# Optimization experiments

Hardware: AMD Instinct MI355X
Metric: run time of the kernel (lower is better)

Reference implementation:

```python
import jax, jax.numpy as jnp
import numpy as np

IN_F = 128
OUT_F = 128
N_LAYER = 2
DEPTH = 9                       # tree depth -> levels 0..DEPTH-1
N_TREES = 128
TREE_SIZE = 2 ** DEPTH - 1      # 511 nodes per complete binary tree
N = N_TREES * TREE_SIZE         # 65408 total nodes
E = N_TREES * (TREE_SIZE - 1)   # 65280 parent->child edges


def _build_forest():
    """Complete binary trees in heap layout; leaves get order 0, root order DEPTH-1."""
    k = np.arange(TREE_SIZE)
    depth = np.floor(np.log2(k + 1)).astype(np.int32)
    order_tree = (DEPTH - 1) - depth                      # per-node level within a tree
    node_order = np.tile(order_tree, N_TREES).astype(np.int32)
    internal = k[k < 2 ** (DEPTH - 1) - 1]                # internal nodes have 2 children
    par = np.repeat(internal, 2)
    chi = np.empty_like(par)
    chi[0::2] = 2 * internal + 1
    chi[1::2] = 2 * internal + 2
    eorder_tree = order_tree[par]
    offs = (np.arange(N_TREES) * TREE_SIZE)[:, None]
    parents = (par[None, :] + offs).reshape(-1)
    children = (chi[None, :] + offs).reshape(-1)
    adjacency = np.stack([parents, children], axis=1).astype(np.int32)
    edge_order = np.tile(eorder_tree, N_TREES).astype(np.int32)
    return node_order, adjacency, edge_order


def setup_inputs() -> dict:
    key = jax.random.key(0)
    ks = jax.random.split(key, 8)
    node_order, adjacency, edge_order = _build_forest()
    s = 0.05
    return {
        "features": jax.random.normal(ks[0], (N, IN_F), jnp.float32),
        "W_iou": jax.random.normal(ks[1], (N_LAYER, 3 * OUT_F, IN_F), jnp.float32) * s,
        "b_iou": jax.random.normal(ks[2], (N_LAYER, 3 * OUT_F), jnp.float32) * s,
        "U_iou": jax.random.normal(ks[3], (N_LAYER, 3 * OUT_F, OUT_F), jnp.float32) * s,
        "W_f": jax.random.normal(ks[4], (N_LAYER, OUT_F, IN_F), jnp.float32) * s,
        "b_f": jax.random.normal(ks[5], (N_LAYER, OUT_F), jnp.float32) * s,
        "U_f": jax.random.normal(ks[6], (N_LAYER, OUT_F, OUT_F), jnp.float32) * s,
        "node_order": jnp.asarray(node_order),
        "adjacency_list": jnp.asarray(adjacency),
        "edge_order": jnp.asarray(edge_order),
        "treesizes": jnp.full((N_TREES,), TREE_SIZE, jnp.int32),
        "n_levels": DEPTH,
    }


def reference(features, W_iou, b_iou, U_iou, W_f, b_f, U_f,
              node_order, adjacency_list, edge_order, treesizes, n_levels):
    n_nodes = features.shape[0]
    parent = adjacency_list[:, 0]
    child = adjacency_list[:, 1]
    n_trees = treesizes.shape[0]
    tree_size = n_nodes // n_trees
    # root of each (equal-sized) tree = argmax of node_order within its segment
    root_idx = (jnp.argmax(node_order.reshape(n_trees, tree_size), axis=1)
                + jnp.arange(n_trees) * tree_size)

    def run_layer(Wi, bi, Ui, Wf, bf, Uf):
        Wx_iou = features @ Wi.T + bi              # [N, 3H], level-independent
        Wfx = features[parent] @ Wf.T + bf         # [E, H], per-edge forget input
        H = Wi.shape[0] // 3

        def step(carry, lvl):
            h, c = carry
            em = (edge_order == lvl).astype(features.dtype)[:, None]   # [E,1]
            ch = h[child]                                              # gather child h
            cc = c[child]
            h_sum = jax.ops.segment_sum(ch * em, parent, num_segments=n_nodes)
            iou = Wx_iou + h_sum @ Ui.T
            i_, o_, u_ = jnp.split(iou, 3, axis=1)
            i_ = jax.nn.sigmoid(i_)
            o_ = jax.nn.sigmoid(o_)
            u_ = jnp.tanh(u_)
            f = jax.nn.sigmoid(Wfx + ch @ Uf.T)                        # [E,H]
            c_sum = jax.ops.segment_sum(f * cc * em, parent, num_segments=n_nodes)
            c_new = i_ * u_ + c_sum
            h_new = o_ * jnp.tanh(c_new)
            nm = (node_order == lvl)[:, None]
            return (jnp.where(nm, h_new, h), jnp.where(nm, c_new, c)), None

        init = (jnp.zeros((n_nodes, H), features.dtype),
                jnp.zeros((n_nodes, H), features.dtype))
        (h, c), _ = jax.lax.scan(step, init, jnp.arange(n_levels))
        return h[root_idx], c[root_idx]

    f_h, f_c = jax.vmap(run_layer)(W_iou, b_iou, U_iou, W_f, b_f, U_f)
    return f_h, f_c
```

## Files before the change

### kernel.cpp

```cpp
#include <hip/hip_runtime.h>
#include <hip/hip_bf16.h>


#define TS 511
#define NT 128
#define NN (NT * TS)

typedef __attribute__((ext_vector_type(8))) short short8;
typedef __attribute__((ext_vector_type(4))) float floatx4;

#define MFMA_B16 __builtin_amdgcn_mfma_f32_16x16x32_bf16

#define BARLDS() do { \
    asm volatile("s_waitcnt lgkmcnt(0)" ::: "memory"); \
    __builtin_amdgcn_s_barrier(); \
    asm volatile("" ::: "memory"); \
} while (0)

__device__ __forceinline__ unsigned short f2b(float f) {
    return __builtin_bit_cast(unsigned short, __float2bfloat16(f));
}
__device__ __forceinline__ float b2f_u(unsigned short u) {
    unsigned v = (unsigned)u << 16;
    return __builtin_bit_cast(float, v);
}
__device__ __forceinline__ float rcp_(float x) { return __builtin_amdgcn_rcpf(x); }
__device__ __forceinline__ float sig_(float x) { return rcp_(1.0f + __expf(-x)); }
__device__ __forceinline__ float tanh_(float x) {
    float a = fabsf(x);
    float t = __expf(-2.0f * a);
    return copysignf((1.0f - t) * rcp_(1.0f + t), x);
}

__global__ void pack_b(const float* __restrict__ Wiou, const float* __restrict__ biou,
                       const float* __restrict__ Uiou, const float* __restrict__ Wf,
                       const float* __restrict__ bfv, const float* __restrict__ Uf,
                       const float* __restrict__ feat,
                       unsigned short* __restrict__ BgU, unsigned short* __restrict__ BgX,
                       float* __restrict__ bp5, unsigned short* __restrict__ xb) {
    int tid = blockIdx.x * 256 + threadIdx.x;
    if (tid < 1280) {
        int l = tid / 640, r = tid % 640, g = r >> 7, o = r & 127;
        bp5[tid] = (g < 3) ? biou[l * 384 + r] : bfv[l * 128 + o];
    }
    if (tid < 131072) {
        int l = tid >> 16, r = tid & 65535, col = r >> 7, kp = r & 127;
        float v = (col < 384) ? Uiou[(l * 384 + col) * 128 + kp]
                              : Uf[(l * 128 + (col - 384)) * 128 + kp];
        BgU[((size_t)(l * 512 + col)) * 128 + kp] = f2b(v);
    } else if (tid < 262144) {
        int e2 = tid - 131072;
        int l = e2 >> 16, r = e2 & 65535, col = r >> 7, kp = r & 127;
        float v = (col < 384) ? Wiou[(l * 384 + col) * 128 + kp]
                              : Wf[(l * 128 + (col - 384)) * 128 + kp];
        BgX[((size_t)(l * 512 + col)) * 128 + kp] = f2b(v);
    } else {
        int e = tid - 262144;
        size_t base = (size_t)e * 8;
        float4 v0 = *(const float4*)(feat + base);
        float4 v1 = *(const float4*)(feat + base + 4);
        short8 r;
        r[0] = (short)f2b(v0.x); r[1] = (short)f2b(v0.y);
        r[2] = (short)f2b(v0.z); r[3] = (short)f2b(v0.w);
        r[4] = (short)f2b(v1.x); r[5] = (short)f2b(v1.y);
        r[6] = (short)f2b(v1.z); r[7] = (short)f2b(v1.w);
        *(short8*)(xb + base) = r;
    }
}

__global__ __launch_bounds__(512, 2) void forest(
        const unsigned short* __restrict__ xb16, const unsigned short* __restrict__ BgU,
        const unsigned short* __restrict__ BgX, const float* __restrict__ bp5,
        float* __restrict__ out) {
    __shared__ __align__(16) unsigned short S[69632];
    const int HC0 = 26112;

    const int tid = threadIdx.x;
    const int l = blockIdx.x >> 7, tree = blockIdx.x & 127;
    const int lane = tid & 63, w = tid >> 6;
    const int quad = lane >> 4, l15 = lane & 15;
    const int o = w * 16 + l15;
    const unsigned short* xb = xb16 + (size_t)tree * TS * 128;
    const unsigned short* BU = BgU + (size_t)l * 512 * 128;
    const unsigned short* BX = BgX + (size_t)l * 512 * 128;

    short8 bU[4][4], bX[4][4];
#pragma unroll
    for (int g = 0; g < 4; g++) {
        const size_t cb = (size_t)(g * 128 + o) * 128;
#pragma unroll
        for (int kbl = 0; kbl < 4; kbl++) {
            bU[g][kbl] = *(const short8*)(BU + cb + kbl * 32 + quad * 8);
            bX[g][kbl] = *(const short8*)(BX + cb + kbl * 32 + quad * 8);
        }
    }
    float bb[5];
#pragma unroll
    for (int g = 0; g < 5; g++) bb[g] = bp5[l * 640 + g * 128 + o];

    auto ldx = [&](int heap, int kbl) -> short8 {
        return *(const short8*)(xb + (size_t)heap * 128 + kbl * 32 + quad * 8);
    };

    auto ltile = [&](int heapA, int selfH, int selfC) {
        floatx4 ai = (floatx4){0.f, 0.f, 0.f, 0.f};
        floatx4 ao = ai, au = ai;
#pragma unroll
        for (int kbl = 0; kbl < 4; kbl++) {
            short8 ax = ldx(heapA, kbl);
            ai = MFMA_B16(ax, bX[0][kbl], ai, 0, 0, 0);
            ao = MFMA_B16(ax, bX[1][kbl], ao, 0, 0, 0);
            au = MFMA_B16(ax, bX[2][kbl], au, 0, 0, 0);
        }
#pragma unroll
        for (int r = 0; r < 4; r++) {
            int idx = quad * 4 + r;
            float iv = sig_(ai[r] + bb[0]);
            float ov = sig_(ao[r] + bb[1]);
            float uv = tanh_(au[r] + bb[2]);
            float cn = iv * uv;
            float hn = ov * tanh_(cn);
            S[(selfH + idx) * 136 + o] = f2b(hn);
            S[HC0 + (selfC + idx) * 136 + o] = f2b(cn);
        }
    };

    auto itile = [&](int heapA, int chAh, int selfRB, int chRBc,
                     int nValid, bool isRoot) {
        floatx4 ai = (floatx4){0.f, 0.f, 0.f, 0.f};
        floatx4 ao = ai, au = ai, awx = ai, af0 = ai, af1 = ai;
#pragma unroll
        for (int kbl = 0; kbl < 4; kbl++) {
            short8 h0 = *(const short8*)&S[chAh * 136 + kbl * 32 + quad * 8];
            short8 h1 = *(const short8*)&S[(chAh + 1) * 136 + kbl * 32 + quad * 8];
            short8 ax = ldx(heapA, kbl);
            ai = MFMA_B16(h0, bU[0][kbl], ai, 0, 0, 0);
            ai = MFMA_B16(h1, bU[0][kbl], ai, 0, 0, 0);
            ao = MFMA_B16(h0, bU[1][kbl], ao, 0, 0, 0);
            ao = MFMA_B16(h1, bU[1][kbl], ao, 0, 0, 0);
            au = MFMA_B16(h0, bU[2][kbl], au, 0, 0, 0);
            au = MFMA_B16(h1, bU[2][kbl], au, 0, 0, 0);
            af0 = MFMA_B16(h0, bU[3][kbl], af0, 0, 0, 0);
            af1 = MFMA_B16(h1, bU[3][kbl], af1, 0, 0, 0);
            ai = MFMA_B16(ax, bX[0][kbl], ai, 0, 0, 0);
            ao = MFMA_B16(ax, bX[1][kbl], ao, 0, 0, 0);
            au = MFMA_B16(ax, bX[2][kbl], au, 0, 0, 0);
            awx = MFMA_B16(ax, bX[3][kbl], awx, 0, 0, 0);
        }
#pragma unroll
        for (int r = 0; r < 4; r++) {
            int idx = quad * 4 + r;
            if (idx < nValid) {
                float iv = sig_(ai[r] + bb[0]);
                float ov = sig_(ao[r] + bb[1]);
                float uv = tanh_(au[r] + bb[2]);
                float f0 = sig_(awx[r] + af0[r] + bb[3]);
                float f1 = sig_(awx[r] + af1[r] + bb[4]);
                float c0 = b2f_u(S[HC0 + (chRBc + 2 * idx) * 136 + o]);
                float c1 = b2f_u(S[HC0 + (chRBc + 2 * idx + 1) * 136 + o]);
                float cn = iv * uv + f0 * c0 + f1 * c1;
                float hn = ov * tanh_(cn);
                S[(selfRB + idx) * 136 + o] = f2b(hn);
                S[HC0 + (selfRB + idx) * 136 + o] = f2b(cn);
                if (isRoot) {
                    out[((size_t)l * 128 + tree) * 128 + o] = hn;
                    out[32768 + ((size_t)l * 128 + tree) * 128 + o] = cn;
                }
            }
        }
    };

#pragma unroll
    for (int s = 0; s < 2; s++)
        ltile(255 + s * 16 + l15, 384 + s * 16, 256 + s * 16);
    BARLDS();

#pragma unroll 2
    for (int t = 0; t < 8; t++) {
        if (t < 7) {
            int b2 = (t + 1) & 1;
#pragma unroll
            for (int s = 0; s < 2; s++)
                ltile(255 + (t + 1) * 32 + s * 16 + l15,
                      384 + b2 * 32 + s * 16, 256 + b2 * 32 + s * 16);
        }
        int b = t & 1;
        itile(127 + t * 16 + l15,
              384 + b * 32 + 2 * l15,
              t * 16,
              256 + b * 32,
              16, false);
        BARLDS();
    }

#pragma unroll
    for (int dd = 6; dd >= 0; dd--) {
        const int nd = 1 << dd;
        const int selfB = (dd == 6) ? 128 : 64 - 2 * nd;
        const int chB = (dd == 6) ? 0 : ((dd == 5) ? 128 : 64 - 4 * nd);
        const int mts = (nd + 15) >> 4;
#pragma unroll
        for (int mt = 0; mt < mts; mt++) {
            int rl = mt * 16 + l15;
            if (rl > nd - 1) rl = nd - 1;
            int nv = nd - mt * 16;
            if (nv > 16) nv = 16;
            itile(nd - 1 + rl,
                  chB + 2 * rl,
                  selfB + mt * 16,
                  chB + 2 * mt * 16,
                  nv, dd == 0);
        }
        BARLDS();
    }
}

extern "C" void kernel_launch(void* const* d_in, const int* in_sizes, int n_in,
                              void* d_out, int out_size, void* d_ws, size_t ws_size,
                              hipStream_t stream) {
    const float* feat = (const float*)d_in[0];
    const float* Wiou = (const float*)d_in[1];
    const float* biou = (const float*)d_in[2];
    const float* Uiou = (const float*)d_in[3];
    const float* Wf   = (const float*)d_in[4];
    const float* bfv  = (const float*)d_in[5];
    const float* Uf   = (const float*)d_in[6];
    float* out = (float*)d_out;

    unsigned short* BgU = (unsigned short*)d_ws;
    unsigned short* BgX = BgU + (size_t)131072;
    unsigned short* xb16 = BgX + (size_t)131072;
    float* bp5 = (float*)(xb16 + (size_t)NN * 128);

    pack_b<<<5112, 256, 0, stream>>>(Wiou, biou, Uiou, Wf, bfv, Uf, feat,
                                     BgU, BgX, bp5, xb16);
    forest<<<256, 512, 0, stream>>>(xb16, BgU, BgX, bp5, out);
}
```

Baseline: 157.6 us.

## Spill depth-7 states to global memory to shrink LDS footprint

The 128 depth-7 node h/c states are now written to a global scratch buffer instead of LDS, and depth 6 reads them back from global. This shrinks LDS use from about 136KB to about 69KB per block and uses a heap-indexed LDS layout for the upper levels. The launch-bound occupancy hint is dropped. The cost is extra global round trips plus a threadfence. With only 256 blocks the grid may not gain much from the smaller LDS footprint.

Result: slower. 206.0 us (+30.7%).

```diff
diff --git a/kernel.cpp b/kernel.cpp
--- a/kernel.cpp
+++ b/kernel.cpp
@@ -68,12 +68,13 @@
     }
 }
 
-__global__ __launch_bounds__(512, 2) void forest(
+__global__ __launch_bounds__(512) void forest(
         const unsigned short* __restrict__ xb16, const unsigned short* __restrict__ BgU,
         const unsigned short* __restrict__ BgX, const float* __restrict__ bp5,
+        unsigned short* __restrict__ hb7, unsigned short* __restrict__ cb7,
         float* __restrict__ out) {
-    __shared__ __align__(16) unsigned short S[69632];
-    const int HC0 = 26112;
+    __shared__ __align__(16) unsigned short S[34544];
+    const int HC0 = 17272;
 
     const int tid = threadIdx.x;
     const int l = blockIdx.x >> 7, tree = blockIdx.x & 127;
@@ -81,6 +82,8 @@
     const int quad = lane >> 4, l15 = lane & 15;
     const int o = w * 16 + l15;
     const unsigned short* xb = xb16 + (size_t)tree * TS * 128;
+    unsigned short* lh = hb7 + ((size_t)(l * 128 + tree)) * 128 * 128;
+    unsigned short* lc = cb7 + ((size_t)(l * 128 + tree)) * 128 * 128;
     const unsigned short* BU = BgU + (size_t)l * 512 * 128;
     const unsigned short* BX = BgX + (size_t)l * 512 * 128;
 
@@ -102,7 +105,7 @@
         return *(const short8*)(xb + (size_t)heap * 128 + kbl * 32 + quad * 8);
     };
 
-    auto ltile = [&](int heapA, int selfH, int selfC) {
+    auto ltile = [&](int heapA, int selfR) {
         floatx4 ai = (floatx4){0.f, 0.f, 0.f, 0.f};
         floatx4 ao = ai, au = ai;
 #pragma unroll
@@ -120,20 +123,20 @@
             float uv = tanh_(au[r] + bb[2]);
             float cn = iv * uv;
             float hn = ov * tanh_(cn);
-            S[(selfH + idx) * 136 + o] = f2b(hn);
-            S[HC0 + (selfC + idx) * 136 + o] = f2b(cn);
-        }
-    };
-
-    auto itile = [&](int heapA, int chAh, int selfRB, int chRBc,
-                     int nValid, bool isRoot) {
+            S[(selfR + idx) * 136 + o] = f2b(hn);
+            S[HC0 + (selfR + idx) * 136 + o] = f2b(cn);
+        }
+    };
+
+    auto d7g = [&](int t, int b) {
+        const int chAh = 63 + b * 32 + 2 * l15;
         floatx4 ai = (floatx4){0.f, 0.f, 0.f, 0.f};
         floatx4 ao = ai, au = ai, awx = ai, af0 = ai, af1 = ai;
 #pragma unroll
         for (int kbl = 0; kbl < 4; kbl++) {
             short8 h0 = *(const short8*)&S[chAh * 136 + kbl * 32 + quad * 8];
             short8 h1 = *(const short8*)&S[(chAh + 1) * 136 + kbl * 32 + quad * 8];
-            short8 ax = ldx(heapA, kbl);
+            short8 ax = ldx(127 + 16 * t + l15, kbl);
             ai = MFMA_B16(h0, bU[0][kbl], ai, 0, 0, 0);
             ai = MFMA_B16(h1, bU[0][kbl], ai, 0, 0, 0);
             ao = MFMA_B16(h0, bU[1][kbl], ao, 0, 0, 0);
@@ -150,18 +153,103 @@
 #pragma unroll
         for (int r = 0; r < 4; r++) {
             int idx = quad * 4 + r;
-            if (idx < nValid) {
+            float iv = sig_(ai[r] + bb[0]);
+            float ov = sig_(ao[r] + bb[1]);
+            float uv = tanh_(au[r] + bb[2]);
+            float f0 = sig_(awx[r] + af0[r] + bb[3]);
+            float f1 = sig_(awx[r] + af1[r] + bb[4]);
+            float c0 = b2f_u(S[HC0 + (63 + b * 32 + 2 * idx) * 136 + o]);
+            float c1 = b2f_u(S[HC0 + (63 + b * 32 + 2 * idx + 1) * 136 + o]);
+            float cn = iv * uv + f0 * c0 + f1 * c1;
+            float hn = ov * tanh_(cn);
+            size_t gi = (size_t)(t * 16 + idx) * 128 + o;
+            lh[gi] = f2b(hn);
+            lc[gi] = f2b(cn);
+        }
+    };
+
+    auto d6g = [&](int j) {
+        const int di0 = 32 * j + 2 * l15;
+        floatx4 ai = (floatx4){0.f, 0.f, 0.f, 0.f};
+        floatx4 ao = ai, au = ai, awx = ai, af0 = ai, af1 = ai;
+#pragma unroll
+        for (int kbl = 0; kbl < 4; kbl++) {
+            short8 h0 = *(const short8*)(lh + (size_t)di0 * 128 + kbl * 32 + quad * 8);
+            short8 h1 = *(const short8*)(lh + (size_t)(di0 + 1) * 128 + kbl * 32 + quad * 8);
+            short8 ax = ldx(63 + 16 * j + l15, kbl);
+            ai = MFMA_B16(h0, bU[0][kbl], ai, 0, 0, 0);
+            ai = MFMA_B16(h1, bU[0][kbl], ai, 0, 0, 0);
+            ao = MFMA_B16(h0, bU[1][kbl], ao, 0, 0, 0);
+            ao = MFMA_B16(h1, bU[1][kbl], ao, 0, 0, 0);
+            au = MFMA_B16(h0, bU[2][kbl], au, 0, 0, 0);
+            au = MFMA_B16(h1, bU[2][kbl], au, 0, 0, 0);
+            af0 = MFMA_B16(h0, bU[3][kbl], af0, 0, 0, 0);
+            af1 = MFMA_B16(h1, bU[3][kbl], af1, 0, 0, 0);
+            ai = MFMA_B16(ax, bX[0][kbl], ai, 0, 0, 0);
+            ao = MFMA_B16(ax, bX[1][kbl], ao, 0, 0, 0);
+            au = MFMA_B16(ax, bX[2][kbl], au, 0, 0, 0);
+            awx = MFMA_B16(ax, bX[3][kbl], awx, 0, 0, 0);
+        }
+#pragma unroll
+        for (int r = 0; r < 4; r++) {
+            int idx = quad * 4 + r;
+            int node = 63 + 16 * j + idx;
+            int dic = 32 * j + 2 * idx;
+            float iv = sig_(ai[r] + bb[0]);
+            float ov = sig_(ao[r] + bb[1]);
+            float uv = tanh_(au[r] + bb[2]);
+            float f0 = sig_(awx[r] + af0[r] + bb[3]);
+            float f1 = sig_(awx[r] + af1[r] + bb[4]);
+            float c0 = b2f_u(lc[(size_t)dic * 128 + o]);
+            float c1 = b2f_u(lc[(size_t)(dic + 1) * 128 + o]);
+            float cn = iv * uv + f0 * c0 + f1 * c1;
+            float hn = ov * tanh_(cn);
+            S[node * 136 + o] = f2b(hn);
+            S[HC0 + node * 136 + o] = f2b(cn);
+        }
+    };
+
+    auto itile_l = [&](int base, int nv, bool isRoot) {
+        const int rl = (l15 < nv) ? l15 : nv - 1;
+        const int nA = base + rl;
+        const int ch0 = 2 * nA + 1;
+        floatx4 ai = (floatx4){0.f, 0.f, 0.f, 0.f};
+        floatx4 ao = ai, au = ai, awx = ai, af0 = ai, af1 = ai;
+#pragma unroll
+        for (int kbl = 0; kbl < 4; kbl++) {
+            short8 h0 = *(const short8*)&S[ch0 * 136 + kbl * 32 + quad * 8];
+            short8 h1 = *(const short8*)&S[(ch0 + 1) * 136 + kbl * 32 + quad * 8];
+            short8 ax = ldx(nA, kbl);
+            ai = MFMA_B16(h0, bU[0][kbl], ai, 0, 0, 0);
+            ai = MFMA_B16(h1, bU[0][kbl], ai, 0, 0, 0);
+            ao = MFMA_B16(h0, bU[1][kbl], ao, 0, 0, 0);
+            ao = MFMA_B16(h1, bU[1][kbl], ao, 0, 0, 0);
+            au = MFMA_B16(h0, bU[2][kbl], au, 0, 0, 0);
+            au = MFMA_B16(h1, bU[2][kbl], au, 0, 0, 0);
+            af0 = MFMA_B16(h0, bU[3][kbl], af0, 0, 0, 0);
+            af1 = MFMA_B16(h1, bU[3][kbl], af1, 0, 0, 0);
+            ai = MFMA_B16(ax, bX[0][kbl], ai, 0, 0, 0);
+            ao = MFMA_B16(ax, bX[1][kbl], ao, 0, 0, 0);
+            au = MFMA_B16(ax, bX[2][kbl], au, 0, 0, 0);
+            awx = MFMA_B16(ax, bX[3][kbl], awx, 0, 0, 0);
+        }
+#pragma unroll
+        for (int r = 0; r < 4; r++) {
+            int idx = quad * 4 + r;
+            if (idx < nv) {
+                int node = base + idx;
+                int ch = 2 * node + 1;
                 float iv = sig_(ai[r] + bb[0]);
                 float ov = sig_(ao[r] + bb[1]);
                 float uv = tanh_(au[r] + bb[2]);
                 float f0 = sig_(awx[r] + af0[r] + bb[3]);
                 float f1 = sig_(awx[r] + af1[r] + bb[4]);
-                float c0 = b2f_u(S[HC0 + (chRBc + 2 * idx) * 136 + o]);
-                float c1 = b2f_u(S[HC0 + (chRBc + 2 * idx + 1) * 136 + o]);
+                float c0 = b2f_u(S[HC0 + ch * 136 + o]);
+                float c1 = b2f_u(S[HC0 + (ch + 1) * 136 + o]);
                 float cn = iv * uv + f0 * c0 + f1 * c1;
                 float hn = ov * tanh_(cn);
-                S[(selfRB + idx) * 136 + o] = f2b(hn);
-                S[HC0 + (selfRB + idx) * 136 + o] = f2b(cn);
+                S[node * 136 + o] = f2b(hn);
+                S[HC0 + node * 136 + o] = f2b(cn);
                 if (isRoot) {
                     out[((size_t)l * 128 + tree) * 128 + o] = hn;
                     out[32768 + ((size_t)l * 128 + tree) * 128 + o] = cn;
@@ -170,49 +258,40 @@
         }
     };
 
-#pragma unroll
-    for (int s = 0; s < 2; s++)
-        ltile(255 + s * 16 + l15, 384 + s * 16, 256 + s * 16);
-    BARLDS();
-
-#pragma unroll 2
+    ltile(255 + l15, 63);
+    ltile(271 + l15, 63 + 16);
+    BARLDS();
+
+#pragma unroll 1
     for (int t = 0; t < 8; t++) {
+        const int b = t & 1;
         if (t < 7) {
-            int b2 = (t + 1) & 1;
-#pragma unroll
-            for (int s = 0; s < 2; s++)
-                ltile(255 + (t + 1) * 32 + s * 16 + l15,
-                      384 + b2 * 32 + s * 16, 256 + b2 * 32 + s * 16);
-        }
-        int b = t & 1;
-        itile(127 + t * 16 + l15,
-              384 + b * 32 + 2 * l15,
-              t * 16,
-              256 + b * 32,
-              16, false);
+            const int b2 = b ^ 1;
+            ltile(287 + 32 * t + l15, 63 + b2 * 32);
+            ltile(303 + 32 * t + l15, 63 + b2 * 32 + 16);
+        }
+        d7g(t, b);
         BARLDS();
     }
 
-#pragma unroll
-    for (int dd = 6; dd >= 0; dd--) {
-        const int nd = 1 << dd;
-        const int selfB = (dd == 6) ? 128 : 64 - 2 * nd;
-        const int chB = (dd == 6) ? 0 : ((dd == 5) ? 128 : 64 - 4 * nd);
-        const int mts = (nd + 15) >> 4;
-#pragma unroll
-        for (int mt = 0; mt < mts; mt++) {
-            int rl = mt * 16 + l15;
-            if (rl > nd - 1) rl = nd - 1;
-            int nv = nd - mt * 16;
-            if (nv > 16) nv = 16;
-            itile(nd - 1 + rl,
-                  chB + 2 * rl,
-                  selfB + mt * 16,
-                  chB + 2 * mt * 16,
-                  nv, dd == 0);
-        }
-        BARLDS();
-    }
+    __threadfence();
+    __syncthreads();
+
+#pragma unroll 2
+    for (int j = 0; j < 4; j++) d6g(j);
+    BARLDS();
+    itile_l(31, 16, false);
+    itile_l(47, 16, false);
+    BARLDS();
+    itile_l(15, 16, false);
+    BARLDS();
+    itile_l(7, 8, false);
+    BARLDS();
+    itile_l(3, 4, false);
+    BARLDS();
+    itile_l(1, 2, false);
+    BARLDS();
+    itile_l(0, 1, true);
 }
 
 extern "C" void kernel_launch(void* const* d_in, const int* in_sizes, int n_in,
@@ -230,9 +309,11 @@
     unsigned short* BgU = (unsigned short*)d_ws;
     unsigned short* BgX = BgU + (size_t)131072;
     unsigned short* xb16 = BgX + (size_t)131072;
-    float* bp5 = (float*)(xb16 + (size_t)NN * 128);
+    unsigned short* hb7 = xb16 + (size_t)NN * 128;
+    unsigned short* cb7 = hb7 + (size_t)4194304;
+    float* bp5 = (float*)(cb7 + (size_t)4194304);
 
     pack_b<<<5112, 256, 0, stream>>>(Wiou, biou, Uiou, Wf, bfv, Uf, feat,
                                      BgU, BgX, bp5, xb16);
-    forest<<<256, 512, 0, stream>>>(xb16, BgU, BgX, bp5, out);
-}
+    forest<<<256, 512, 0, stream>>>(xb16, BgU, BgX, bp5, hb7, cb7, out);
+}
```
